# Kernel optimization log

Hardware: AMD Instinct MI355X
Metric: run time of the kernel (lower is better)

Reference implementation:

```python
import jax, jax.numpy as jnp
import numpy as np

N, E, H = 50000, 500000, 4
DIN, DH, DO, TD = 135, 128, 64, 9

def _ln(x, g, b):
    mu = jnp.mean(x, axis=-1, keepdims=True)
    v = jnp.var(x, axis=-1, keepdims=True)
    return (x - mu) / jnp.sqrt(v + 1e-5) * g + b

def _gat(x, src, dst, W, a_src, a_dst, b, n, heads, c):
    h = (x @ W).reshape(n, heads, c)                      # [N,H,C]
    es = jnp.sum(h * a_src, -1)                           # [N,H]
    ed = jnp.sum(h * a_dst, -1)
    e = jax.nn.leaky_relu(es[src] + ed[dst], 0.2)         # [E,H]
    m = jax.ops.segment_max(e, dst, num_segments=n)       # segment softmax over dst
    ex = jnp.exp(e - m[dst])
    den = jax.ops.segment_sum(ex, dst, num_segments=n)
    alpha = ex / (den[dst] + 1e-16)
    out = jax.ops.segment_sum(h[src] * alpha[..., None], dst, num_segments=n)
    return jnp.mean(out, axis=1) + b                      # concat=False -> head mean

def setup_inputs() -> dict:
    key = jax.random.key(0)
    ks = jax.random.split(key, 32)
    rn = lambda i, shape: jax.random.normal(ks[i], shape, jnp.float32) * 0.05
    inp = {}
    inp['x'] = jax.random.normal(ks[0], (N, DIN), jnp.float32)
    inp['edge_index'] = jax.random.randint(ks[1], (2, E), 0, N, jnp.int32)
    inp['edge_attr'] = jnp.ones((E, 1), jnp.float32)
    inp['W_in'] = rn(2, (DIN, DH)); inp['b_in'] = jnp.zeros((DH,), jnp.float32)
    inp['g1W'] = rn(3, (DH, H * DH)); inp['g1as'] = rn(4, (H, DH)); inp['g1ad'] = rn(5, (H, DH)); inp['g1b'] = jnp.zeros((DH,), jnp.float32)
    inp['g2W'] = rn(6, (DH, H * DH)); inp['g2as'] = rn(7, (H, DH)); inp['g2ad'] = rn(8, (H, DH)); inp['g2b'] = jnp.zeros((DH,), jnp.float32)
    inp['g3W'] = rn(9, (DH, H * DO)); inp['g3as'] = rn(10, (H, DO)); inp['g3ad'] = rn(11, (H, DO)); inp['g3b'] = jnp.zeros((DO,), jnp.float32)
    inp['r1W'] = rn(12, (DH, DH)); inp['r1b'] = jnp.zeros((DH,), jnp.float32)
    inp['r2W'] = rn(13, (DH, DH)); inp['r2b'] = jnp.zeros((DH,), jnp.float32)
    inp['r3W'] = rn(14, (DH, DO)); inp['r3b'] = jnp.zeros((DO,), jnp.float32)
    inp['n1g'] = jnp.ones((DH,), jnp.float32); inp['n1b'] = jnp.zeros((DH,), jnp.float32)
    inp['n2g'] = jnp.ones((DH,), jnp.float32); inp['n2b'] = jnp.zeros((DH,), jnp.float32)
    inp['n3g'] = jnp.ones((DO,), jnp.float32); inp['n3b'] = jnp.zeros((DO,), jnp.float32)
    inp['tw'] = jnp.float32(0.3)
    inp['c1W'] = rn(15, (DO, DO)); inp['c1b'] = jnp.zeros((DO,), jnp.float32)
    inp['clg'] = jnp.ones((DO,), jnp.float32); inp['clb'] = jnp.zeros((DO,), jnp.float32)
    inp['c2W'] = rn(16, (DO, 2)); inp['c2b'] = jnp.zeros((2,), jnp.float32)
    return inp

def reference(x, edge_index, edge_attr, W_in, b_in, g1W, g1as, g1ad, g1b,
              g2W, g2as, g2ad, g2b, g3W, g3as, g3ad, g3b,
              r1W, r1b, r2W, r2b, r3W, r3b,
              n1g, n1b, n2g, n2b, n3g, n3b, tw,
              c1W, c1b, clg, clb, c2W, c2b):
    n = x.shape[0]
    src0, dst0 = edge_index[0], edge_index[1]
    loop = jnp.arange(n, dtype=edge_index.dtype)          # GATConv add_self_loops=True
    src = jnp.concatenate([src0, loop])
    dst = jnp.concatenate([dst0, loop])
    # vectorized temporal cosine similarity over original edges
    t = x[:, -TD:]
    ti, tj = t[src0], t[dst0]
    nrm = jnp.maximum(jnp.linalg.norm(ti, axis=-1), 1e-8) * jnp.maximum(jnp.linalg.norm(tj, axis=-1), 1e-8)
    sim = jnp.sum(ti * tj, -1) / nrm
    scale = 1.0 + 0.1 * jnp.mean(1.0 + tw * sim)
    h = x @ W_in + b_in
    id1 = h
    h = _gat(h, src, dst, g1W, g1as, g1ad, g1b, n, H, DH) * scale
    h = _ln(jax.nn.relu(h) + id1 @ r1W + r1b, n1g, n1b)
    id2 = h
    h = _gat(h, src, dst, g2W, g2as, g2ad, g2b, n, H, DH) * scale
    h = _ln(jax.nn.relu(h) + id2 @ r2W + r2b, n2g, n2b)
    id3 = h
    h = _gat(h, src, dst, g3W, g3as, g3ad, g3b, n, H, DO)
    h = _ln(jax.nn.relu(h) + id3 @ r3W + r3b, n3g, n3b)
    ego = h[0:1]
    z = jax.nn.relu(ego @ c1W + c1b)
    z = _ln(z, clg, clb)
    return z @ c2W + c2b
```

## Files before the change

### kernel.cpp

```cpp
#include <hip/hip_runtime.h>

#define AGENT __HIP_MEMORY_SCOPE_AGENT

constexpr int TD = 9, TDP = 12, DIN = 135;
constexpr int CAPD = 64;
constexpr int CAP3 = 256, CAP2 = 1024, CAP1 = 4096;
constexpr int NBM = 512;
constexpr int LSTRIDE = 32;
constexpr int NGRP = 16, GSZ = NBM / NGRP;
constexpr int NSET = 8;
constexpr int NLINE = 64;
constexpr int PB = 8;
constexpr int NGC = CAP1 / PB;

struct P {
  const float* x; const int* src; const int* dst; int N; int E;
  const float *W_in,*b_in,*g1W,*g1as,*g1ad,*g1b,*g2W,*g2as,*g2ad,*g2b,*g3W,*g3as,*g3ad,*g3b;
  const float *r1W,*r1b,*r2W,*r2b,*r3W,*r3b,*n1g,*n1b,*n2g,*n2b,*n3g,*n3b;
  const float *tw,*c1W,*c1b,*clg,*clb,*c2W,*c2b;
  float* tp;
  int *deg, *bk;
  int *m3,*m2,*m1,*list3,*list2,*list1,*cnts;
  int *barc,*barr,*barg;
  int *fc,*fd,*fe;
  float *h0,*hh1,*es1,*ed1,*h1,*hh2,*es2,*ed2,*h2,*hh3,*es3,*ed3,*h3;
  float* dout;
};

__device__ __forceinline__ float lrelu(float v) { return v >= 0.f ? v : 0.2f * v; }

__device__ __forceinline__ void stg(float* pp, float v) { __hip_atomic_store(pp, v, __ATOMIC_RELAXED, AGENT); }
__device__ __forceinline__ void stg(int* pp, int v)   { __hip_atomic_store(pp, v, __ATOMIC_RELAXED, AGENT); }

__device__ __forceinline__ void spinf(const int* f) {
  while (__hip_atomic_load((int*)f, __ATOMIC_RELAXED, AGENT) == 0) __builtin_amdgcn_s_sleep(2);
}

__device__ __forceinline__ bool claim_node(int v, int* __restrict__ m, int* __restrict__ list,
                                           int* __restrict__ cnt, int cap) {
  if (atomicCAS(&m[v], -1, -2) == -1) {
    int pos = atomicAdd(cnt, 1);
    if (pos < cap) { stg(&list[pos], v); stg(&m[v], pos); } else { stg(&m[v], -3); }
    return true;
  }
  return false;
}

__device__ __forceinline__ void mid_barrier(const P& p, int& lgen, int* amroot_s) {
  __syncthreads();
  int g = lgen + 1;
  if (threadIdx.x == 0) {
    *amroot_s = 0;
    int* gc = &p.barc[(((g & (NSET - 1)) * NGRP) + (blockIdx.x & (NGRP - 1))) * LSTRIDE];
    if (__hip_atomic_fetch_add(gc, 1, __ATOMIC_RELAXED, AGENT) == GSZ - 1) {
      int* rc = &p.barr[(g & (NSET - 1)) * LSTRIDE];
      if (__hip_atomic_fetch_add(rc, 1, __ATOMIC_RELAXED, AGENT) == NGRP - 1) *amroot_s = 1;
    }
  }
  __syncthreads();
  if (*amroot_s) {
    if (threadIdx.x < NLINE)
      __hip_atomic_store(&p.barg[threadIdx.x * LSTRIDE], g, __ATOMIC_RELAXED, AGENT);
  } else if (threadIdx.x == 0) {
    int* line = &p.barg[(blockIdx.x & (NLINE - 1)) * LSTRIDE];
    while (__hip_atomic_load(line, __ATOMIC_RELAXED, AGENT) < g)
      __builtin_amdgcn_s_sleep(8);
  }
  __syncthreads();
  lgen = g;
}

__global__ void k_prep(P p) {
  int gt = blockIdx.x * blockDim.x + threadIdx.x;
  int GT = gridDim.x * blockDim.x;
  int n3 = 3 * p.N;
  int4* mv = (int4*)p.m3;
  int4 neg = make_int4(-1, -1, -1, -1);
  int nv = n3 >> 2;
  for (int i = gt; i < nv; i += GT) mv[i] = neg;
  for (int i = (nv << 2) + gt; i < n3; i += GT) p.m3[i] = -1;
  int4* dv = (int4*)p.deg;
  int4 z4 = make_int4(0, 0, 0, 0);
  int ndv = p.N >> 2;
  for (int i = gt; i < ndv; i += GT) dv[i] = z4;
  for (int i = (ndv << 2) + gt; i < p.N; i += GT) p.deg[i] = 0;
  if (gt < 64) p.cnts[gt] = 0;
  for (int i = gt; i < NSET * NGRP * LSTRIDE; i += GT) p.barc[i] = 0;
  for (int i = gt; i < NSET * LSTRIDE; i += GT) p.barr[i] = 0;
  for (int i = gt; i < NLINE * LSTRIDE; i += GT) p.barg[i] = 0;
  for (int i = gt; i < NGC; i += GT) p.fc[i] = 0;
  for (int i = gt; i < CAP2; i += GT) p.fd[i] = 0;
  for (int i = gt; i < CAP3; i += GT) p.fe[i] = 0;
  int total = p.N * TDP;
  for (int i = gt; i < total; i += GT) {
    int v = i / TDP, k = i - v * TDP;
    p.tp[i] = (k < TD) ? p.x[(size_t)v * DIN + (DIN - TD) + k] : 0.f;
  }
}

__global__ void k_scan(P p) {
  __shared__ float wred[4];
  int tid = threadIdx.x;
  int gt = blockIdx.x * blockDim.x + tid, GT = gridDim.x * blockDim.x;
  if (gt == 0) claim_node(0, p.m3, p.list3, &p.cnts[0], CAP3);
  const float4* t4 = (const float4*)p.tp;
  float local = 0.f;
  auto edge_proc = [&](int s, int d) {
    int slot = atomicAdd(&p.deg[d], 1);
    if (slot < CAPD) p.bk[(size_t)d * CAPD + slot] = s;
    if (d == 0) claim_node(s, p.m3, p.list3, &p.cnts[0], CAP3);
    float4 a0 = t4[s * 3], a1 = t4[s * 3 + 1], a2 = t4[s * 3 + 2];
    float4 b0 = t4[d * 3], b1 = t4[d * 3 + 1], b2 = t4[d * 3 + 2];
    float dot = a0.x*b0.x + a0.y*b0.y + a0.z*b0.z + a0.w*b0.w
              + a1.x*b1.x + a1.y*b1.y + a1.z*b1.z + a1.w*b1.w
              + a2.x*b2.x;
    float na = a0.x*a0.x + a0.y*a0.y + a0.z*a0.z + a0.w*a0.w
             + a1.x*a1.x + a1.y*a1.y + a1.z*a1.z + a1.w*a1.w
             + a2.x*a2.x;
    float nb = b0.x*b0.x + b0.y*b0.y + b0.z*b0.z + b0.w*b0.w
             + b1.x*b1.x + b1.y*b1.y + b1.z*b1.z + b1.w*b1.w
             + b2.x*b2.x;
    local += dot / (fmaxf(sqrtf(na), 1e-8f) * fmaxf(sqrtf(nb), 1e-8f));
  };
  int nq4 = p.E >> 2;
  const int4* s4p = (const int4*)p.src;
  const int4* d4p = (const int4*)p.dst;
  for (int q = gt; q < nq4; q += GT) {
    int4 s4 = s4p[q], d4 = d4p[q];
    edge_proc(s4.x, d4.x); edge_proc(s4.y, d4.y); edge_proc(s4.z, d4.z); edge_proc(s4.w, d4.w);
  }
  for (int e = (nq4 << 2) + gt; e < p.E; e += GT) edge_proc(p.src[e], p.dst[e]);
  for (int off = 32; off > 0; off >>= 1) local += __shfl_down(local, off, 64);
  if ((tid & 63) == 0) wred[tid >> 6] = local;
  __syncthreads();
  if (tid == 0) atomicAdd((float*)&p.cnts[8], wred[0] + wred[1] + wred[2] + wred[3]);
}

template <int C, int ONEXT, int FDIV>
__device__ void gat_flag(const P& p, int q, const int* lst, const int* mPrev,
                         const int* flagIn, int* flagOut,
                         const float* hh, const float* es, const float* ed, const float* hres,
                         const float* gb, const float* rW, const float* rb,
                         const float* ng, const float* nbv, float scale,
                         float* hout, const float* Wn, const float* avn, const float* bvn,
                         float* hhn, float* esn, float* edn,
                         float* elog, int* eposs, float* ev_s, float* sh,
                         float* hres_s, float* shln, float* psn, float* pdn, float* sc2) {
  const int Wd = 4 * C, R = Wd / 256;
  int tid = threadIdx.x;
  int v = lst[q];
  int sp = mPrev[v];
  int nb = min(p.deg[v], CAPD);
  if (tid == 0) spinf(&flagIn[max(sp, 0) / FDIV]);
  for (int j = tid; j < nb; j += 256) {
    int pu = mPrev[p.bk[(size_t)v * CAPD + j]];
    eposs[j] = pu;
    spinf(&flagIn[max(pu, 0) / FDIV]);
  }
  __syncthreads();
  for (int j = tid; j < nb; j += 256) {
    int pu = eposs[j];
    const float* ep = &es[(size_t)pu * 4];
    elog[0 * CAPD + j] = ep[0]; elog[1 * CAPD + j] = ep[1];
    elog[2 * CAPD + j] = ep[2]; elog[3 * CAPD + j] = ep[3];
  }
  if (tid < 4) { ev_s[tid] = es[(size_t)sp * 4 + tid]; ev_s[4 + tid] = ed[(size_t)sp * 4 + tid]; }
  for (int k = tid; k < 128; k += 256) hres_s[k] = hres[(size_t)sp * 128 + k];
  __syncthreads();
#pragma unroll
  for (int r = 0; r < R; r++) {
    int w = r * 256 + tid, a = w / C;
    float edv = ev_s[4 + a];
    float eself = lrelu(ev_s[a] + edv);
    float mx = eself;
    for (int j = 0; j < nb; j++) mx = fmaxf(mx, lrelu(elog[a * CAPD + j] + edv));
    float den = __expf(eself - mx);
    for (int j = 0; j < nb; j++) den += __expf(lrelu(elog[a * CAPD + j] + edv) - mx);
    float rden = 1.f / (den + 1e-16f);
    float s = __expf(eself - mx) * rden * hh[(size_t)sp * Wd + w];
    for (int j = 0; j < nb; j++)
      s += __expf(lrelu(elog[a * CAPD + j] + edv) - mx) * rden * hh[(size_t)eposs[j] * Wd + w];
    sh[w] = s;
  }
  __syncthreads();
  float val = 0.f;
  if (tid < C) {
    float g = 0.25f * (sh[tid] + sh[C + tid] + sh[2 * C + tid] + sh[3 * C + tid]) + gb[tid];
    g *= scale;
    g = fmaxf(g, 0.f);
    float rr = rb[tid];
    for (int k = 0; k < 128; k++) rr += hres_s[k] * rW[(size_t)k * C + tid];
    val = g + rr;
    shln[tid] = val;
  }
  __syncthreads();
  if (tid == 0) {
    float s1 = 0.f, s2 = 0.f;
    for (int k = 0; k < C; k++) { float u = shln[k]; s1 += u; s2 += u * u; }
    float mu = s1 / (float)C;
    sc2[0] = mu;
    sc2[1] = rsqrtf(fmaxf(s2 / (float)C - mu * mu, 0.f) + 1e-5f);
  }
  __syncthreads();
  if (tid < C) {
    float o = (val - sc2[0]) * sc2[1] * ng[tid] + nbv[tid];
    stg(&hout[(size_t)q * C + tid], o);
    shln[tid] = o;
  }
  __syncthreads();
  if (ONEXT > 0) {
    for (int j = tid; j < ONEXT; j += 256) {
      float a2 = 0.f;
      for (int k = 0; k < C; k++) a2 += shln[k] * Wn[(size_t)k * ONEXT + j];
      stg(&hhn[(size_t)q * ONEXT + j], a2);
      psn[j] = a2 * avn[j]; pdn[j] = a2 * bvn[j];
    }
    __syncthreads();
    if (tid < 8) {
      const int CN = ONEXT / 4; int a = tid & 3;
      const float* pr = (tid < 4) ? psn : pdn;
      float s = 0.f;
      for (int cc = 0; cc < CN; cc++) s += pr[a * CN + cc];
      stg(&(tid < 4 ? esn : edn)[(size_t)q * 4 + a], s);
    }
  }
  __syncthreads();
  if (tid == 0 && flagOut) stg(&flagOut[q], 1);
}

__global__ __launch_bounds__(256, 2) void k_mid(P p) {
  __shared__ float xs8[PB][DIN];
  __shared__ float hs8[PB][128];
  __shared__ float psn[512], pdn[512];
  __shared__ int   vid8[PB];
  __shared__ float elog[4 * CAPD];
  __shared__ int   eposs[CAPD];
  __shared__ float ev_s[8], sc2[2];
  __shared__ float sh[512], hres_s[128], shln[128];
  __shared__ float zcl[64];
  __shared__ int   amroot_s;
  __shared__ int   shw;

  int tid = threadIdx.x, bid = blockIdx.x;
  int lgen = 0;
  float scale = 1.1f + 0.1f * p.tw[0] *
      __int_as_float(__hip_atomic_load(&p.cnts[8], __ATOMIC_RELAXED, AGENT)) / (float)p.E;

  {
    int c3 = min(__hip_atomic_load(&p.cnts[0], __ATOMIC_RELAXED, AGENT), CAP3);
    for (int q = bid; q < c3; q += NBM) {
      int v = p.list3[q];
      if (tid == 0) shw = claim_node(v, p.m2, p.list2, &p.cnts[1], CAP2) ? 1 : 0;
      __syncthreads();
      int nb = min(p.deg[v], CAPD);
      for (int j = tid; j < nb; j += 256) {
        int u = p.bk[(size_t)v * CAPD + j];
        if (claim_node(u, p.m2, p.list2, &p.cnts[1], CAP2)) {
          claim_node(u, p.m1, p.list1, &p.cnts[2], CAP1);
          int nbu = min(p.deg[u], CAPD);
          for (int k2 = 0; k2 < nbu; k2++)
            claim_node(p.bk[(size_t)u * CAPD + k2], p.m1, p.list1, &p.cnts[2], CAP1);
        }
      }
      if (shw) {
        if (tid == 0) claim_node(v, p.m1, p.list1, &p.cnts[2], CAP1);
        for (int j = tid; j < nb; j += 256)
          claim_node(p.bk[(size_t)v * CAPD + j], p.m1, p.list1, &p.cnts[2], CAP1);
      }
      __syncthreads();
    }
  }
  mid_barrier(p, lgen, &amroot_s);

  int c1 = min(__hip_atomic_load(&p.cnts[2], __ATOMIC_RELAXED, AGENT), CAP1);
  int c2 = min(__hip_atomic_load(&p.cnts[1], __ATOMIC_RELAXED, AGENT), CAP2);
  int c3 = min(__hip_atomic_load(&p.cnts[0], __ATOMIC_RELAXED, AGENT), CAP3);

  {
    int ngp = (c1 + PB - 1) / PB;
    for (int g = bid; g < ngp; g += NBM) {
      int base = g * PB, nn = min(PB, c1 - base);
      if (tid < nn) vid8[tid] = p.list1[base + tid];
      __syncthreads();
      for (int idx = tid; idx < nn * DIN; idx += 256) {
        int u = idx / DIN, k = idx - u * DIN;
        xs8[u][k] = p.x[(size_t)vid8[u] * DIN + k];
      }
      __syncthreads();
      if (tid < 128) {
        float a[PB]; float bi = p.b_in[tid];
#pragma unroll
        for (int u = 0; u < PB; u++) a[u] = bi;
        for (int k = 0; k < DIN; k++) {
          float w = p.W_in[(size_t)k * 128 + tid];
#pragma unroll
          for (int u = 0; u < PB; u++) a[u] += xs8[u][k] * w;
        }
#pragma unroll
        for (int u = 0; u < PB; u++) {
          hs8[u][tid] = a[u];
          if (u < nn) stg(&p.h0[(size_t)(base + u) * 128 + tid], a[u]);
        }
      }
      __syncthreads();
      float bsv[2][PB];
#pragma unroll
      for (int jj = 0; jj < 2; jj++) {
        int j = jj * 256 + tid;
        float b[PB];
#pragma unroll
        for (int u = 0; u < PB; u++) b[u] = 0.f;
        for (int k = 0; k < 128; k++) {
          float w = p.g1W[(size_t)k * 512 + j];
#pragma unroll
          for (int u = 0; u < PB; u++) b[u] += hs8[u][k] * w;
        }
#pragma unroll
        for (int u = 0; u < PB; u++) {
          bsv[jj][u] = b[u];
          if (u < nn) stg(&p.hh1[(size_t)(base + u) * 512 + j], b[u]);
        }
      }
      for (int u = 0; u < nn; u++) {
#pragma unroll
        for (int jj = 0; jj < 2; jj++) {
          int j = jj * 256 + tid;
          psn[j] = bsv[jj][u] * p.g1as[j];
          pdn[j] = bsv[jj][u] * p.g1ad[j];
        }
        __syncthreads();
        if (tid < 8) {
          int a = tid & 3;
          const float* pr = (tid < 4) ? psn : pdn;
          float s = 0.f;
          for (int cc = 0; cc < 128; cc++) s += pr[a * 128 + cc];
          stg(&(tid < 4 ? p.es1 : p.ed1)[(size_t)(base + u) * 4 + a], s);
        }
        __syncthreads();
      }
      if (tid == 0) stg(&p.fc[g], 1);
    }
  }

  for (int q = bid; q < c2; q += NBM)
    gat_flag<128, 512, PB>(p, q, p.list2, p.m1, p.fc, p.fd,
                           p.hh1, p.es1, p.ed1, p.h0,
                           p.g1b, p.r1W, p.r1b, p.n1g, p.n1b, scale,
                           p.h1, p.g2W, p.g2as, p.g2ad, p.hh2, p.es2, p.ed2,
                           elog, eposs, ev_s, sh, hres_s, shln, psn, pdn, sc2);

  for (int q = bid; q < c3; q += NBM)
    gat_flag<128, 256, 1>(p, q, p.list3, p.m2, p.fd, p.fe,
                          p.hh2, p.es2, p.ed2, p.h1,
                          p.g2b, p.r2W, p.r2b, p.n2g, p.n2b, scale,
                          p.h2, p.g3W, p.g3as, p.g3ad, p.hh3, p.es3, p.ed3,
                          elog, eposs, ev_s, sh, hres_s, shln, psn, pdn, sc2);

  if (bid == 0) {
    int zero = 0;
    gat_flag<64, 0, 1>(p, 0, &zero, p.m3, p.fe, nullptr,
                       p.hh3, p.es3, p.ed3, p.h2,
                       p.g3b, p.r3W, p.r3b, p.n3g, p.n3b, 1.f,
                       p.h3, nullptr, nullptr, nullptr, nullptr, nullptr, nullptr,
                       elog, eposs, ev_s, sh, hres_s, shln, psn, pdn, sc2);
    if (tid < 64) {
      float az = p.c1b[tid];
      for (int k = 0; k < 64; k++) az += shln[k] * p.c1W[k * 64 + tid];
      zcl[tid] = fmaxf(az, 0.f);
    }
    __syncthreads();
    if (tid == 0) {
      float s1 = 0.f, s2 = 0.f;
      for (int k = 0; k < 64; k++) { float u = zcl[k]; s1 += u; s2 += u * u; }
      float mu = s1 / 64.f;
      float rstd = rsqrtf(fmaxf(s2 / 64.f - mu * mu, 0.f) + 1e-5f);
      float o0 = p.c2b[0], o1 = p.c2b[1];
      for (int k = 0; k < 64; k++) {
        float zn = (zcl[k] - mu) * rstd * p.clg[k] + p.clb[k];
        o0 += zn * p.c2W[k * 2 + 0];
        o1 += zn * p.c2W[k * 2 + 1];
      }
      p.dout[0] = o0; p.dout[1] = o1;
    }
  }
}

extern "C" void kernel_launch(void* const* d_in, const int* in_sizes, int n_in,
                              void* d_out, int out_size, void* d_ws, size_t ws_size,
                              hipStream_t stream) {
  P p;
  p.x = (const float*)d_in[0];
  const int* ei = (const int*)d_in[1];
  p.N = in_sizes[0] / DIN;
  p.E = in_sizes[1] / 2;
  p.src = ei; p.dst = ei + p.E;
  p.W_in = (const float*)d_in[3]; p.b_in = (const float*)d_in[4];
  p.g1W = (const float*)d_in[5]; p.g1as = (const float*)d_in[6]; p.g1ad = (const float*)d_in[7]; p.g1b = (const float*)d_in[8];
  p.g2W = (const float*)d_in[9]; p.g2as = (const float*)d_in[10]; p.g2ad = (const float*)d_in[11]; p.g2b = (const float*)d_in[12];
  p.g3W = (const float*)d_in[13]; p.g3as = (const float*)d_in[14]; p.g3ad = (const float*)d_in[15]; p.g3b = (const float*)d_in[16];
  p.r1W = (const float*)d_in[17]; p.r1b = (const float*)d_in[18];
  p.r2W = (const float*)d_in[19]; p.r2b = (const float*)d_in[20];
  p.r3W = (const float*)d_in[21]; p.r3b = (const float*)d_in[22];
  p.n1g = (const float*)d_in[23]; p.n1b = (const float*)d_in[24];
  p.n2g = (const float*)d_in[25]; p.n2b = (const float*)d_in[26];
  p.n3g = (const float*)d_in[27]; p.n3b = (const float*)d_in[28];
  p.tw  = (const float*)d_in[29];
  p.c1W = (const float*)d_in[30]; p.c1b = (const float*)d_in[31];
  p.clg = (const float*)d_in[32]; p.clb = (const float*)d_in[33];
  p.c2W = (const float*)d_in[34]; p.c2b = (const float*)d_in[35];
  p.dout = (float*)d_out;

  char* B = (char*)d_ws;
  size_t off = 0;
  auto take = [&](size_t nbytes) -> char* {
    char* r = B + off;
    off += (nbytes + 255) & ~(size_t)255;
    return r;
  };
  p.cnts  = (int*)take(256);
  p.barc  = (int*)take((size_t)NSET * NGRP * LSTRIDE * 4);
  p.barr  = (int*)take((size_t)NSET * LSTRIDE * 4);
  p.barg  = (int*)take((size_t)NLINE * LSTRIDE * 4);
  p.fc    = (int*)take(NGC * 4);
  p.fd    = (int*)take(CAP2 * 4);
  p.fe    = (int*)take(CAP3 * 4);
  p.m3    = (int*)take((size_t)3 * p.N * 4);
  p.m2 = p.m3 + p.N; p.m1 = p.m2 + p.N;
  p.tp    = (float*)take((size_t)p.N * TDP * 4);
  p.deg   = (int*)take((size_t)p.N * 4);
  p.bk    = (int*)take((size_t)p.N * CAPD * 4);
  p.list3 = (int*)take(CAP3 * 4);
  p.list2 = (int*)take(CAP2 * 4);
  p.list1 = (int*)take(CAP1 * 4);
  p.h0    = (float*)take((size_t)CAP1 * 128 * 4);
  p.hh1   = (float*)take((size_t)CAP1 * 512 * 4);
  p.es1   = (float*)take((size_t)CAP1 * 16);
  p.ed1   = (float*)take((size_t)CAP1 * 16);
  p.h1    = (float*)take((size_t)CAP2 * 128 * 4);
  p.hh2   = (float*)take((size_t)CAP2 * 512 * 4);
  p.es2   = (float*)take((size_t)CAP2 * 16);
  p.ed2   = (float*)take((size_t)CAP2 * 16);
  p.h2    = (float*)take((size_t)CAP3 * 128 * 4);
  p.hh3   = (float*)take((size_t)CAP3 * 256 * 4);
  p.es3   = (float*)take((size_t)CAP3 * 16);
  p.ed3   = (float*)take((size_t)CAP3 * 16);
  p.h3    = (float*)take(64 * 4);

  k_prep<<<1024, 256, 0, stream>>>(p);
  k_scan<<<1024, 256, 0, stream>>>(p);
  k_mid<<<NBM, 256, 0, stream>>>(p);
}
```

Measured before the change: 143.8 us.

## Fuse edge scan into persistent kernel and replace per-item flags with grid barriers

Moves the edge scan (degree bucketing, ego-neighbour claiming, temporal cosine sum) from its own launch into the start of the persistent kernel, followed by a grid barrier. It also replaces the fine-grained per-node ready flags between GAT layers with full grid barriers, which removes the flag zeroing and spin loads. This saves one kernel launch and the flag polling, but gives up the overlap between layers that the dataflow flags allowed. The scan now runs on 512 blocks instead of 1024.

```diff
diff --git a/kernel.cpp b/kernel.cpp
--- a/kernel.cpp
+++ b/kernel.cpp
@@ -11,7 +11,6 @@
 constexpr int NSET = 8;
 constexpr int NLINE = 64;
 constexpr int PB = 8;
-constexpr int NGC = CAP1 / PB;
 
 struct P {
   const float* x; const int* src; const int* dst; int N; int E;
@@ -22,7 +21,6 @@
   int *deg, *bk;
   int *m3,*m2,*m1,*list3,*list2,*list1,*cnts;
   int *barc,*barr,*barg;
-  int *fc,*fd,*fe;
   float *h0,*hh1,*es1,*ed1,*h1,*hh2,*es2,*ed2,*h2,*hh3,*es3,*ed3,*h3;
   float* dout;
 };
@@ -31,10 +29,6 @@
 
 __device__ __forceinline__ void stg(float* pp, float v) { __hip_atomic_store(pp, v, __ATOMIC_RELAXED, AGENT); }
 __device__ __forceinline__ void stg(int* pp, int v)   { __hip_atomic_store(pp, v, __ATOMIC_RELAXED, AGENT); }
-
-__device__ __forceinline__ void spinf(const int* f) {
-  while (__hip_atomic_load((int*)f, __ATOMIC_RELAXED, AGENT) == 0) __builtin_amdgcn_s_sleep(2);
-}
 
 __device__ __forceinline__ bool claim_node(int v, int* __restrict__ m, int* __restrict__ list,
                                            int* __restrict__ cnt, int cap) {
@@ -88,9 +82,6 @@
   for (int i = gt; i < NSET * NGRP * LSTRIDE; i += GT) p.barc[i] = 0;
   for (int i = gt; i < NSET * LSTRIDE; i += GT) p.barr[i] = 0;
   for (int i = gt; i < NLINE * LSTRIDE; i += GT) p.barg[i] = 0;
-  for (int i = gt; i < NGC; i += GT) p.fc[i] = 0;
-  for (int i = gt; i < CAP2; i += GT) p.fd[i] = 0;
-  for (int i = gt; i < CAP3; i += GT) p.fe[i] = 0;
   int total = p.N * TDP;
   for (int i = gt; i < total; i += GT) {
     int v = i / TDP, k = i - v * TDP;
@@ -98,68 +89,23 @@
   }
 }
 
-__global__ void k_scan(P p) {
-  __shared__ float wred[4];
-  int tid = threadIdx.x;
-  int gt = blockIdx.x * blockDim.x + tid, GT = gridDim.x * blockDim.x;
-  if (gt == 0) claim_node(0, p.m3, p.list3, &p.cnts[0], CAP3);
-  const float4* t4 = (const float4*)p.tp;
-  float local = 0.f;
-  auto edge_proc = [&](int s, int d) {
-    int slot = atomicAdd(&p.deg[d], 1);
-    if (slot < CAPD) p.bk[(size_t)d * CAPD + slot] = s;
-    if (d == 0) claim_node(s, p.m3, p.list3, &p.cnts[0], CAP3);
-    float4 a0 = t4[s * 3], a1 = t4[s * 3 + 1], a2 = t4[s * 3 + 2];
-    float4 b0 = t4[d * 3], b1 = t4[d * 3 + 1], b2 = t4[d * 3 + 2];
-    float dot = a0.x*b0.x + a0.y*b0.y + a0.z*b0.z + a0.w*b0.w
-              + a1.x*b1.x + a1.y*b1.y + a1.z*b1.z + a1.w*b1.w
-              + a2.x*b2.x;
-    float na = a0.x*a0.x + a0.y*a0.y + a0.z*a0.z + a0.w*a0.w
-             + a1.x*a1.x + a1.y*a1.y + a1.z*a1.z + a1.w*a1.w
-             + a2.x*a2.x;
-    float nb = b0.x*b0.x + b0.y*b0.y + b0.z*b0.z + b0.w*b0.w
-             + b1.x*b1.x + b1.y*b1.y + b1.z*b1.z + b1.w*b1.w
-             + b2.x*b2.x;
-    local += dot / (fmaxf(sqrtf(na), 1e-8f) * fmaxf(sqrtf(nb), 1e-8f));
-  };
-  int nq4 = p.E >> 2;
-  const int4* s4p = (const int4*)p.src;
-  const int4* d4p = (const int4*)p.dst;
-  for (int q = gt; q < nq4; q += GT) {
-    int4 s4 = s4p[q], d4 = d4p[q];
-    edge_proc(s4.x, d4.x); edge_proc(s4.y, d4.y); edge_proc(s4.z, d4.z); edge_proc(s4.w, d4.w);
-  }
-  for (int e = (nq4 << 2) + gt; e < p.E; e += GT) edge_proc(p.src[e], p.dst[e]);
-  for (int off = 32; off > 0; off >>= 1) local += __shfl_down(local, off, 64);
-  if ((tid & 63) == 0) wred[tid >> 6] = local;
-  __syncthreads();
-  if (tid == 0) atomicAdd((float*)&p.cnts[8], wred[0] + wred[1] + wred[2] + wred[3]);
-}
-
-template <int C, int ONEXT, int FDIV>
-__device__ void gat_flag(const P& p, int q, const int* lst, const int* mPrev,
-                         const int* flagIn, int* flagOut,
-                         const float* hh, const float* es, const float* ed, const float* hres,
-                         const float* gb, const float* rW, const float* rb,
-                         const float* ng, const float* nbv, float scale,
-                         float* hout, const float* Wn, const float* avn, const float* bvn,
-                         float* hhn, float* esn, float* edn,
-                         float* elog, int* eposs, float* ev_s, float* sh,
-                         float* hres_s, float* shln, float* psn, float* pdn, float* sc2) {
+template <int C, int ONEXT>
+__device__ void gat_q(const P& p, int q, const int* lst, const int* mPrev,
+                      const float* hh, const float* es, const float* ed, const float* hres,
+                      const float* gb, const float* rW, const float* rb,
+                      const float* ng, const float* nbv, float scale,
+                      float* hout, const float* Wn, const float* avn, const float* bvn,
+                      float* hhn, float* esn, float* edn,
+                      float* elog, int* eposs, float* ev_s, float* sh,
+                      float* hres_s, float* shln, float* psn, float* pdn, float* sc2) {
   const int Wd = 4 * C, R = Wd / 256;
   int tid = threadIdx.x;
   int v = lst[q];
   int sp = mPrev[v];
   int nb = min(p.deg[v], CAPD);
-  if (tid == 0) spinf(&flagIn[max(sp, 0) / FDIV]);
   for (int j = tid; j < nb; j += 256) {
     int pu = mPrev[p.bk[(size_t)v * CAPD + j]];
     eposs[j] = pu;
-    spinf(&flagIn[max(pu, 0) / FDIV]);
-  }
-  __syncthreads();
-  for (int j = tid; j < nb; j += 256) {
-    int pu = eposs[j];
     const float* ep = &es[(size_t)pu * 4];
     elog[0 * CAPD + j] = ep[0]; elog[1 * CAPD + j] = ep[1];
     elog[2 * CAPD + j] = ep[2]; elog[3 * CAPD + j] = ep[3];
@@ -177,10 +123,10 @@
     float den = __expf(eself - mx);
     for (int j = 0; j < nb; j++) den += __expf(lrelu(elog[a * CAPD + j] + edv) - mx);
     float rden = 1.f / (den + 1e-16f);
-    float s = __expf(eself - mx) * rden * hh[(size_t)sp * Wd + w];
+    float sv = __expf(eself - mx) * rden * hh[(size_t)sp * Wd + w];
     for (int j = 0; j < nb; j++)
-      s += __expf(lrelu(elog[a * CAPD + j] + edv) - mx) * rden * hh[(size_t)eposs[j] * Wd + w];
-    sh[w] = s;
+      sv += __expf(lrelu(elog[a * CAPD + j] + edv) - mx) * rden * hh[(size_t)eposs[j] * Wd + w];
+    sh[w] = sv;
   }
   __syncthreads();
   float val = 0.f;
@@ -219,16 +165,15 @@
     if (tid < 8) {
       const int CN = ONEXT / 4; int a = tid & 3;
       const float* pr = (tid < 4) ? psn : pdn;
-      float s = 0.f;
-      for (int cc = 0; cc < CN; cc++) s += pr[a * CN + cc];
-      stg(&(tid < 4 ? esn : edn)[(size_t)q * 4 + a], s);
-    }
-  }
-  __syncthreads();
-  if (tid == 0 && flagOut) stg(&flagOut[q], 1);
-}
-
-__global__ __launch_bounds__(256, 2) void k_mid(P p) {
+      float sv = 0.f;
+      for (int cc = 0; cc < CN; cc++) sv += pr[a * CN + cc];
+      stg(&(tid < 4 ? esn : edn)[(size_t)q * 4 + a], sv);
+    }
+  }
+  __syncthreads();
+}
+
+__global__ __launch_bounds__(256, 2) void k_mega(P p) {
   __shared__ float xs8[PB][DIN];
   __shared__ float hs8[PB][128];
   __shared__ float psn[512], pdn[512];
@@ -238,13 +183,49 @@
   __shared__ float ev_s[8], sc2[2];
   __shared__ float sh[512], hres_s[128], shln[128];
   __shared__ float zcl[64];
+  __shared__ float wred[4];
   __shared__ int   amroot_s;
   __shared__ int   shw;
 
   int tid = threadIdx.x, bid = blockIdx.x;
+  int gt = bid * 256 + tid, GT = NBM * 256;
   int lgen = 0;
-  float scale = 1.1f + 0.1f * p.tw[0] *
-      __int_as_float(__hip_atomic_load(&p.cnts[8], __ATOMIC_RELAXED, AGENT)) / (float)p.E;
+
+  {
+    if (gt == 0) claim_node(0, p.m3, p.list3, &p.cnts[0], CAP3);
+    const float4* t4 = (const float4*)p.tp;
+    float local = 0.f;
+    auto edge_proc = [&](int s, int d) {
+      int slot = atomicAdd(&p.deg[d], 1);
+      if (slot < CAPD) stg(&p.bk[(size_t)d * CAPD + slot], s);
+      if (d == 0) claim_node(s, p.m3, p.list3, &p.cnts[0], CAP3);
+      float4 a0 = t4[s * 3], a1 = t4[s * 3 + 1], a2 = t4[s * 3 + 2];
+      float4 b0 = t4[d * 3], b1 = t4[d * 3 + 1], b2 = t4[d * 3 + 2];
+      float dot = a0.x*b0.x + a0.y*b0.y + a0.z*b0.z + a0.w*b0.w
+                + a1.x*b1.x + a1.y*b1.y + a1.z*b1.z + a1.w*b1.w
+                + a2.x*b2.x;
+      float na = a0.x*a0.x + a0.y*a0.y + a0.z*a0.z + a0.w*a0.w
+               + a1.x*a1.x + a1.y*a1.y + a1.z*a1.z + a1.w*a1.w
+               + a2.x*a2.x;
+      float nb = b0.x*b0.x + b0.y*b0.y + b0.z*b0.z + b0.w*b0.w
+               + b1.x*b1.x + b1.y*b1.y + b1.z*b1.z + b1.w*b1.w
+               + b2.x*b2.x;
+      local += dot / (fmaxf(sqrtf(na), 1e-8f) * fmaxf(sqrtf(nb), 1e-8f));
+    };
+    int nq4 = p.E >> 2;
+    const int4* s4p = (const int4*)p.src;
+    const int4* d4p = (const int4*)p.dst;
+    for (int q = gt; q < nq4; q += GT) {
+      int4 s4 = s4p[q], d4 = d4p[q];
+      edge_proc(s4.x, d4.x); edge_proc(s4.y, d4.y); edge_proc(s4.z, d4.z); edge_proc(s4.w, d4.w);
+    }
+    for (int e = (nq4 << 2) + gt; e < p.E; e += GT) edge_proc(p.src[e], p.dst[e]);
+    for (int off = 32; off > 0; off >>= 1) local += __shfl_down(local, off, 64);
+    if ((tid & 63) == 0) wred[tid >> 6] = local;
+    __syncthreads();
+    if (tid == 0) atomicAdd((float*)&p.cnts[8], wred[0] + wred[1] + wred[2] + wred[3]);
+  }
+  mid_barrier(p, lgen, &amroot_s);
 
   {
     int c3 = min(__hip_atomic_load(&p.cnts[0], __ATOMIC_RELAXED, AGENT), CAP3);
@@ -275,6 +256,8 @@
   int c1 = min(__hip_atomic_load(&p.cnts[2], __ATOMIC_RELAXED, AGENT), CAP1);
   int c2 = min(__hip_atomic_load(&p.cnts[1], __ATOMIC_RELAXED, AGENT), CAP2);
   int c3 = min(__hip_atomic_load(&p.cnts[0], __ATOMIC_RELAXED, AGENT), CAP3);
+  float scale = 1.1f + 0.1f * p.tw[0] *
+      __int_as_float(__hip_atomic_load(&p.cnts[8], __ATOMIC_RELAXED, AGENT)) / (float)p.E;
 
   {
     int ngp = (c1 + PB - 1) / PB;
@@ -338,31 +321,30 @@
         }
         __syncthreads();
       }
-      if (tid == 0) stg(&p.fc[g], 1);
-    }
-  }
+    }
+  }
+  mid_barrier(p, lgen, &amroot_s);
 
   for (int q = bid; q < c2; q += NBM)
-    gat_flag<128, 512, PB>(p, q, p.list2, p.m1, p.fc, p.fd,
-                           p.hh1, p.es1, p.ed1, p.h0,
-                           p.g1b, p.r1W, p.r1b, p.n1g, p.n1b, scale,
-                           p.h1, p.g2W, p.g2as, p.g2ad, p.hh2, p.es2, p.ed2,
-                           elog, eposs, ev_s, sh, hres_s, shln, psn, pdn, sc2);
+    gat_q<128, 512>(p, q, p.list2, p.m1, p.hh1, p.es1, p.ed1, p.h0,
+                    p.g1b, p.r1W, p.r1b, p.n1g, p.n1b, scale,
+                    p.h1, p.g2W, p.g2as, p.g2ad, p.hh2, p.es2, p.ed2,
+                    elog, eposs, ev_s, sh, hres_s, shln, psn, pdn, sc2);
+  mid_barrier(p, lgen, &amroot_s);
 
   for (int q = bid; q < c3; q += NBM)
-    gat_flag<128, 256, 1>(p, q, p.list3, p.m2, p.fd, p.fe,
-                          p.hh2, p.es2, p.ed2, p.h1,
-                          p.g2b, p.r2W, p.r2b, p.n2g, p.n2b, scale,
-                          p.h2, p.g3W, p.g3as, p.g3ad, p.hh3, p.es3, p.ed3,
-                          elog, eposs, ev_s, sh, hres_s, shln, psn, pdn, sc2);
+    gat_q<128, 256>(p, q, p.list3, p.m2, p.hh2, p.es2, p.ed2, p.h1,
+                    p.g2b, p.r2W, p.r2b, p.n2g, p.n2b, scale,
+                    p.h2, p.g3W, p.g3as, p.g3ad, p.hh3, p.es3, p.ed3,
+                    elog, eposs, ev_s, sh, hres_s, shln, psn, pdn, sc2);
+  mid_barrier(p, lgen, &amroot_s);
 
   if (bid == 0) {
     int zero = 0;
-    gat_flag<64, 0, 1>(p, 0, &zero, p.m3, p.fe, nullptr,
-                       p.hh3, p.es3, p.ed3, p.h2,
-                       p.g3b, p.r3W, p.r3b, p.n3g, p.n3b, 1.f,
-                       p.h3, nullptr, nullptr, nullptr, nullptr, nullptr, nullptr,
-                       elog, eposs, ev_s, sh, hres_s, shln, psn, pdn, sc2);
+    gat_q<64, 0>(p, 0, &zero, p.m3, p.hh3, p.es3, p.ed3, p.h2,
+                 p.g3b, p.r3W, p.r3b, p.n3g, p.n3b, 1.f,
+                 p.h3, nullptr, nullptr, nullptr, nullptr, nullptr, nullptr,
+                 elog, eposs, ev_s, sh, hres_s, shln, psn, pdn, sc2);
     if (tid < 64) {
       float az = p.c1b[tid];
       for (int k = 0; k < 64; k++) az += shln[k] * p.c1W[k * 64 + tid];
@@ -421,9 +403,6 @@
   p.barc  = (int*)take((size_t)NSET * NGRP * LSTRIDE * 4);
   p.barr  = (int*)take((size_t)NSET * LSTRIDE * 4);
   p.barg  = (int*)take((size_t)NLINE * LSTRIDE * 4);
-  p.fc    = (int*)take(NGC * 4);
-  p.fd    = (int*)take(CAP2 * 4);
-  p.fe    = (int*)take(CAP3 * 4);
   p.m3    = (int*)take((size_t)3 * p.N * 4);
   p.m2 = p.m3 + p.N; p.m1 = p.m2 + p.N;
   p.tp    = (float*)take((size_t)p.N * TDP * 4);
@@ -447,6 +426,5 @@
   p.h3    = (float*)take(64 * 4);
 
   k_prep<<<1024, 256, 0, stream>>>(p);
-  k_scan<<<1024, 256, 0, stream>>>(p);
-  k_mid<<<NBM, 256, 0, stream>>>(p);
-}
+  k_mega<<<NBM, 256, 0, stream>>>(p);
+}
```

Measured after the change: 145.1 us. No clear change (+0.8%).
